# Kernel tuning notes

Hardware: AMD Instinct MI355X
Metric: run time of the kernel (lower is better)

Reference implementation:

```python
import jax, jax.numpy as jnp
import numpy as np

N, D, C = 4096, 512, 100
EPS = 1e-8


def setup_inputs() -> dict:
    key = jax.random.key(0)
    k1, k2 = jax.random.split(key)
    X = jax.random.normal(k1, (N, D), dtype=jnp.float32)
    # torch.rand -> uniform [0, 1), shape (1, hiddensize, classes)
    grp = jax.random.uniform(k2, (1, D, C), dtype=jnp.float32)
    return {"X": X, "grp": grp}


def reference(X, grp):
    # L1 distance of each sample to each class prototype: [N, D, 1] - [1, D, C] -> sum over D -> [N, C]
    l1 = jnp.abs(X[:, :, None] - grp).sum(axis=1)
    norm = jax.nn.softmax(-l1, axis=1)  # Softmin over classes

    # Cosine similarity between X [N, D] and prototypes grp[0] [D, C] -> [N, C]
    g = grp[0]
    dot = X @ g  # [N, C]
    xn = jnp.sqrt(jnp.sum(X * X, axis=1, keepdims=True))      # [N, 1]
    gn = jnp.sqrt(jnp.sum(g * g, axis=0, keepdims=True))      # [1, C]
    cs = dot / jnp.maximum(xn * gn, EPS)

    confidence = jnp.max(cs, axis=1, keepdims=True)  # [N, 1]
    confusion = jax.nn.softmax(cs, axis=1)           # [N, C]
    return confidence * confusion * norm
```

## Files before the change

kernel.cpp:

```cpp
#include <hip/hip_runtime.h>

#define D_DIM 512
#define C_CLS 100
#define SAMP 8
#define NT 256

__global__ __launch_bounds__(128) void gn_kernel(const float* __restrict__ grp,
                                                 float* __restrict__ gn) {
    __shared__ float4 red[128];
    const int t = threadIdx.x;
    const int cb = blockIdx.x * 4;
    float4 acc = {0.f, 0.f, 0.f, 0.f};
    for (int d = t; d < D_DIM; d += 128) {
        float4 g = *(const float4*)&grp[d * C_CLS + cb];
        acc.x = fmaf(g.x, g.x, acc.x);
        acc.y = fmaf(g.y, g.y, acc.y);
        acc.z = fmaf(g.z, g.z, acc.z);
        acc.w = fmaf(g.w, g.w, acc.w);
    }
    red[t] = acc;
    __syncthreads();
    for (int off = 64; off > 0; off >>= 1) {
        if (t < off) {
            float4 a = red[t], b = red[t + off];
            a.x += b.x; a.y += b.y; a.z += b.z; a.w += b.w;
            red[t] = a;
        }
        __syncthreads();
    }
    if (t == 0) {
        float4 a = red[0];
        gn[cb + 0] = sqrtf(a.x);
        gn[cb + 1] = sqrtf(a.y);
        gn[cb + 2] = sqrtf(a.z);
        gn[cb + 3] = sqrtf(a.w);
    }
}

__global__ __launch_bounds__(NT) void cls_kernel(const float* __restrict__ X,
                                                 const float* __restrict__ grp,
                                                 const float* __restrict__ gn,
                                                 float* __restrict__ out) {
    __shared__ float xs[SAMP][520];
    __shared__ float part[4][2][25][36];
    __shared__ float redA[SAMP][25];
    __shared__ float redB[SAMP][25];

    const int t = threadIdx.x;
    const int n0 = blockIdx.x * SAMP;

    {
        const float4* Xv = (const float4*)(X + (size_t)n0 * D_DIM);
        for (int i = t; i < SAMP * D_DIM / 4; i += NT) {
            int row = i >> 7;
            int col = i & 127;
            *(float4*)&xs[row][col * 4] = Xv[i];
        }
    }
    __syncthreads();

    const bool act = (t < 200);
    int dq = 0, sg = 0, cq = 0;
    if (act) { dq = t / 50; int r = t % 50; sg = r / 25; cq = r % 25; }

    float l1[4][4];
    float dt[4][4];
    float xq[4];
#pragma unroll
    for (int i = 0; i < 4; ++i) {
        xq[i] = 0.f;
#pragma unroll
        for (int j = 0; j < 4; ++j) { l1[i][j] = 0.f; dt[i][j] = 0.f; }
    }

    if (act) {
        const float* gp = grp + cq * 4;
        const int dbase = dq * 128;
        for (int dd = 0; dd < 128; dd += 4) {
            const int d4 = dbase + dd;
            float xr[4][4];
#pragma unroll
            for (int si = 0; si < 4; ++si)
                *(float4*)&xr[si][0] = *(const float4*)&xs[sg * 4 + si][d4];
#pragma unroll
            for (int k = 0; k < 4; ++k) {
                float4 g = *(const float4*)&gp[(d4 + k) * C_CLS];
                float ga[4] = {g.x, g.y, g.z, g.w};
#pragma unroll
                for (int si = 0; si < 4; ++si) {
                    float x = xr[si][k];
                    xq[si] = fmaf(x, x, xq[si]);
#pragma unroll
                    for (int c = 0; c < 4; ++c) {
                        l1[si][c] += fabsf(x - ga[c]);
                        dt[si][c] = fmaf(x, ga[c], dt[si][c]);
                    }
                }
            }
        }
        float* p = &part[dq][sg][cq][0];
#pragma unroll
        for (int si = 0; si < 4; ++si) {
            *(float4*)&p[si * 4]      = *(float4*)&l1[si][0];
            *(float4*)&p[16 + si * 4] = *(float4*)&dt[si][0];
        }
        *(float4*)&p[32] = *(float4*)&xq[0];
    }
    __syncthreads();

    const int s  = t / 25;
    const int c2 = t - s * 25;
    const bool act2 = (t < 200);

    float l1c[4] = {0.f, 0.f, 0.f, 0.f};
    float dtc[4] = {0.f, 0.f, 0.f, 0.f};
    float xsq = 0.f;
    if (act2) {
        const int sg2 = s >> 2, si2 = s & 3;
#pragma unroll
        for (int q = 0; q < 4; ++q) {
            const float* p = &part[q][sg2][c2][0];
            float4 a = *(const float4*)&p[si2 * 4];
            float4 b = *(const float4*)&p[16 + si2 * 4];
            l1c[0] += a.x; l1c[1] += a.y; l1c[2] += a.z; l1c[3] += a.w;
            dtc[0] += b.x; dtc[1] += b.y; dtc[2] += b.z; dtc[3] += b.w;
            xsq += p[32 + si2];
        }
    }

    float cs[4] = {0.f, 0.f, 0.f, 0.f};
    if (act2) {
        float xn = sqrtf(xsq);
        float4 gv = *(const float4*)&gn[c2 * 4];
        cs[0] = dtc[0] / fmaxf(xn * gv.x, 1e-8f);
        cs[1] = dtc[1] / fmaxf(xn * gv.y, 1e-8f);
        cs[2] = dtc[2] / fmaxf(xn * gv.z, 1e-8f);
        cs[3] = dtc[3] / fmaxf(xn * gv.w, 1e-8f);
        redA[s][c2] = fminf(fminf(l1c[0], l1c[1]), fminf(l1c[2], l1c[3]));
        redB[s][c2] = fmaxf(fmaxf(cs[0], cs[1]), fmaxf(cs[2], cs[3]));
    }
    __syncthreads();

    float minl1 = 0.f, maxcs = 0.f;
    if (act2) {
        minl1 = redA[s][0];
        maxcs = redB[s][0];
        for (int k = 1; k < 25; ++k) {
            minl1 = fminf(minl1, redA[s][k]);
            maxcs = fmaxf(maxcs, redB[s][k]);
        }
    }
    __syncthreads();

    if (act2) {
        redA[s][c2] = __expf(minl1 - l1c[0]) + __expf(minl1 - l1c[1]) +
                      __expf(minl1 - l1c[2]) + __expf(minl1 - l1c[3]);
        redB[s][c2] = __expf(cs[0] - maxcs) + __expf(cs[1] - maxcs) +
                      __expf(cs[2] - maxcs) + __expf(cs[3] - maxcs);
    }
    __syncthreads();

    if (act2) {
        float s1 = 0.f, s2 = 0.f;
        for (int k = 0; k < 25; ++k) { s1 += redA[s][k]; s2 += redB[s][k]; }
        float f = maxcs / (s1 * s2);
        float4 o;
        o.x = f * __expf(cs[0] - maxcs) * __expf(minl1 - l1c[0]);
        o.y = f * __expf(cs[1] - maxcs) * __expf(minl1 - l1c[1]);
        o.z = f * __expf(cs[2] - maxcs) * __expf(minl1 - l1c[2]);
        o.w = f * __expf(cs[3] - maxcs) * __expf(minl1 - l1c[3]);
        *(float4*)&out[(size_t)(n0 + s) * C_CLS + c2 * 4] = o;
    }
}

extern "C" void kernel_launch(void* const* d_in, const int* in_sizes, int n_in,
                              void* d_out, int out_size, void* d_ws, size_t ws_size,
                              hipStream_t stream) {
    const float* X   = (const float*)d_in[0];
    const float* grp = (const float*)d_in[1];
    float* out = (float*)d_out;
    float* gn  = (float*)d_ws;

    gn_kernel<<<25, 128, 0, stream>>>(grp, gn);
    cls_kernel<<<4096 / SAMP, NT, 0, stream>>>(X, grp, gn, out);
}
```

Before: 36.67 us.

## Halve samples per block, split D eight ways, compute row norms separately

Each block now handles 4 samples instead of 8, doubling the grid to 1024 blocks. The 200 worker threads now split the D dimension into 8 chunks of 64 rather than 4 chunks across two sample groups. The per-row squared norm leaves the inner loop and is computed up front with a wave shuffle reduction. Launch bounds now request 4 blocks per CU, and the reduction stage uses 100 threads. This aims for more parallelism and occupancy and less inner-loop work, at the cost of loading each prototype column twice as often and a larger cross-chunk reduction.

```diff
diff --git a/kernel.cpp b/kernel.cpp
--- a/kernel.cpp
+++ b/kernel.cpp
@@ -2,7 +2,7 @@
 
 #define D_DIM 512
 #define C_CLS 100
-#define SAMP 8
+#define SAMP 4
 #define NT 256
 
 __global__ __launch_bounds__(128) void gn_kernel(const float* __restrict__ grp,
@@ -37,20 +37,22 @@
     }
 }
 
-__global__ __launch_bounds__(NT) void cls_kernel(const float* __restrict__ X,
-                                                 const float* __restrict__ grp,
-                                                 const float* __restrict__ gn,
-                                                 float* __restrict__ out) {
+__global__ __launch_bounds__(NT, 4) void cls_kernel(const float* __restrict__ X,
+                                                    const float* __restrict__ grp,
+                                                    const float* __restrict__ gn,
+                                                    float* __restrict__ out) {
     __shared__ float xs[SAMP][520];
-    __shared__ float part[4][2][25][36];
+    __shared__ float part[8][25][36];
     __shared__ float redA[SAMP][25];
     __shared__ float redB[SAMP][25];
+    __shared__ float xsqs[SAMP];
 
     const int t = threadIdx.x;
     const int n0 = blockIdx.x * SAMP;
 
     {
         const float4* Xv = (const float4*)(X + (size_t)n0 * D_DIM);
+#pragma unroll
         for (int i = t; i < SAMP * D_DIM / 4; i += NT) {
             int row = i >> 7;
             int col = i & 127;
@@ -59,29 +61,40 @@
     }
     __syncthreads();
 
+    if (t < 128) {
+        const int r = t >> 5, j = t & 31;
+        float v = 0.f;
+#pragma unroll
+        for (int k = 0; k < 4; ++k) {
+            float4 a = *(const float4*)&xs[r][j * 4 + k * 128];
+            v += a.x * a.x + a.y * a.y + a.z * a.z + a.w * a.w;
+        }
+#pragma unroll
+        for (int m = 16; m > 0; m >>= 1) v += __shfl_xor(v, m, 32);
+        if (j == 0) xsqs[r] = v;
+    }
+
     const bool act = (t < 200);
-    int dq = 0, sg = 0, cq = 0;
-    if (act) { dq = t / 50; int r = t % 50; sg = r / 25; cq = r % 25; }
+    const int dq = t / 25;
+    const int cq = t - dq * 25;
 
     float l1[4][4];
     float dt[4][4];
-    float xq[4];
 #pragma unroll
-    for (int i = 0; i < 4; ++i) {
-        xq[i] = 0.f;
+    for (int i = 0; i < 4; ++i)
 #pragma unroll
         for (int j = 0; j < 4; ++j) { l1[i][j] = 0.f; dt[i][j] = 0.f; }
-    }
 
     if (act) {
         const float* gp = grp + cq * 4;
-        const int dbase = dq * 128;
-        for (int dd = 0; dd < 128; dd += 4) {
+        const int dbase = dq * 64;
+#pragma unroll 4
+        for (int dd = 0; dd < 64; dd += 4) {
             const int d4 = dbase + dd;
             float xr[4][4];
 #pragma unroll
             for (int si = 0; si < 4; ++si)
-                *(float4*)&xr[si][0] = *(const float4*)&xs[sg * 4 + si][d4];
+                *(float4*)&xr[si][0] = *(const float4*)&xs[si][d4];
 #pragma unroll
             for (int k = 0; k < 4; ++k) {
                 float4 g = *(const float4*)&gp[(d4 + k) * C_CLS];
@@ -89,7 +102,6 @@
 #pragma unroll
                 for (int si = 0; si < 4; ++si) {
                     float x = xr[si][k];
-                    xq[si] = fmaf(x, x, xq[si]);
 #pragma unroll
                     for (int c = 0; c < 4; ++c) {
                         l1[si][c] += fabsf(x - ga[c]);
@@ -98,39 +110,35 @@
                 }
             }
         }
-        float* p = &part[dq][sg][cq][0];
+        float* p = &part[dq][cq][0];
 #pragma unroll
         for (int si = 0; si < 4; ++si) {
             *(float4*)&p[si * 4]      = *(float4*)&l1[si][0];
             *(float4*)&p[16 + si * 4] = *(float4*)&dt[si][0];
         }
-        *(float4*)&p[32] = *(float4*)&xq[0];
     }
     __syncthreads();
 
     const int s  = t / 25;
     const int c2 = t - s * 25;
-    const bool act2 = (t < 200);
+    const bool act2 = (t < 100);
 
     float l1c[4] = {0.f, 0.f, 0.f, 0.f};
     float dtc[4] = {0.f, 0.f, 0.f, 0.f};
-    float xsq = 0.f;
     if (act2) {
-        const int sg2 = s >> 2, si2 = s & 3;
 #pragma unroll
-        for (int q = 0; q < 4; ++q) {
-            const float* p = &part[q][sg2][c2][0];
-            float4 a = *(const float4*)&p[si2 * 4];
-            float4 b = *(const float4*)&p[16 + si2 * 4];
+        for (int q = 0; q < 8; ++q) {
+            const float* p = &part[q][c2][0];
+            float4 a = *(const float4*)&p[s * 4];
+            float4 b = *(const float4*)&p[16 + s * 4];
             l1c[0] += a.x; l1c[1] += a.y; l1c[2] += a.z; l1c[3] += a.w;
             dtc[0] += b.x; dtc[1] += b.y; dtc[2] += b.z; dtc[3] += b.w;
-            xsq += p[32 + si2];
         }
     }
 
     float cs[4] = {0.f, 0.f, 0.f, 0.f};
     if (act2) {
-        float xn = sqrtf(xsq);
+        float xn = sqrtf(xsqs[s]);
         float4 gv = *(const float4*)&gn[c2 * 4];
         cs[0] = dtc[0] / fmaxf(xn * gv.x, 1e-8f);
         cs[1] = dtc[1] / fmaxf(xn * gv.y, 1e-8f);
```

After: 35.91 us. 2.1% less time.
